# Optimization experiments

Hardware: AMD Instinct MI355X
Metric: run time of the kernel (lower is better)

## Reference

```python
import jax, jax.numpy as jnp
import numpy as np

B, E, H, W = 8, 256, 128, 128
E0 = E1 = E2 = E3 = E // 4  # channel_split=[2,2,2,2] -> equal quarters


def _dwconv(x, w, b, dilation, padding):
    # x: [B,C,H,W], w: [C,1,kh,kw] (OIHW, feature_group_count=C), b: [C]
    C = x.shape[1]
    y = jax.lax.conv_general_dilated(
        x, w,
        window_strides=(1, 1),
        padding=[(padding, padding), (padding, padding)],
        rhs_dilation=(dilation, dilation),
        feature_group_count=C,
        dimension_numbers=("NCHW", "OIHW", "NCHW"))
    return y + b[None, :, None, None]


def setup_inputs() -> dict:
    key = jax.random.key(0)
    ks = jax.random.split(key, 9)
    s = 0.05
    return {
        "x": jax.random.normal(ks[0], (B, E, H, W), dtype=jnp.float32),
        "w0": jax.random.normal(ks[1], (E, 1, 3, 3), dtype=jnp.float32) * s,
        "b0": jax.random.normal(ks[2], (E,), dtype=jnp.float32) * s,
        "w1": jax.random.normal(ks[3], (E1, 1, 3, 3), dtype=jnp.float32) * s,
        "b1": jax.random.normal(ks[4], (E1,), dtype=jnp.float32) * s,
        "w2": jax.random.normal(ks[5], (E2, 1, 5, 5), dtype=jnp.float32) * s,
        "b2": jax.random.normal(ks[6], (E2,), dtype=jnp.float32) * s,
        "w_pw": jax.random.normal(ks[7], (E, E), dtype=jnp.float32) * s,
        "b_pw": jax.random.normal(ks[8], (E,), dtype=jnp.float32) * s,
    }


def reference(x, w0, b0, w1, b1, w2, b2, w_pw, b_pw):
    # Stage 1: full-width 3x3 depthwise, dilation 1, padding 1
    x0 = _dwconv(x, w0, b0, dilation=1, padding=1)
    # Branch convs on channel slices of x0 (note: original code applies
    # DW_conv2 to BOTH the 3rd and 4th slices; DW_conv3 is never used).
    x1 = _dwconv(x0[:, E0:E0 + E1], w1, b1, dilation=3, padding=3)          # 3x3 dil3
    x2 = _dwconv(x0[:, E0 + E1:E0 + E1 + E2], w2, b2, dilation=3, padding=6)  # 5x5 dil3
    x3 = _dwconv(x0[:, E - E3:], w2, b2, dilation=3, padding=6)             # reuses DW_conv2
    xc = jnp.concatenate([x0[:, :E0], x1, x2, x3], axis=1)  # [B,E,H,W]
    # 1x1 pointwise conv as a channel GEMM
    y = jnp.einsum("bchw,oc->bohw", xc, w_pw) + b_pw[None, :, None, None]
    return y
```

## Files before the change

kernel.cpp:

```cpp
#include <hip/hip_runtime.h>

typedef _Float16 f16;
typedef _Float16 f16x8 __attribute__((ext_vector_type(8)));
typedef unsigned short u16x8 __attribute__((ext_vector_type(8)));
typedef float f32x4 __attribute__((ext_vector_type(4)));

#define GLB_AS(p) ((const __attribute__((address_space(1))) unsigned int*)(p))
#define LDS_AS(p) ((__attribute__((address_space(3))) unsigned int*)(p))

__global__ __launch_bounds__(256) void whalf(const float* __restrict__ w,
                                             f16* __restrict__ wh) {
  int i = blockIdx.x * 256 + threadIdx.x;
  wh[i] = (f16)w[i];
}

template <int HT>
__global__ __launch_bounds__(256) void dwfuse(
    const float* __restrict__ x, const float* __restrict__ w0,
    const float* __restrict__ b0, const float* __restrict__ w1,
    const float* __restrict__ b1, const float* __restrict__ w2,
    const float* __restrict__ b2, f16* __restrict__ Xp) {
  constexpr int S2 = 32 + 2 * HT;
  constexpr int S1 = S2 + 2;
  constexpr int PO = (HT == 6) ? 2 : 0;
  constexpr int QW = (S2 + 3) / 4;
  constexpr int LW = 52;
  __shared__ float xs[S1 * LW];
  __shared__ float ts[S2 * LW];
  const int tid = threadIdx.x;

  int b, ch;
  if constexpr (HT == 0) { b = blockIdx.z >> 6; ch = (int)(blockIdx.z & 63); }
  else if constexpr (HT == 3) { b = blockIdx.z >> 6; ch = 64 + (int)(blockIdx.z & 63); }
  else { b = blockIdx.z >> 7; ch = 128 + (int)(blockIdx.z & 127); }
  const int plane = b * 256 + ch;
  const int R0 = (int)blockIdx.y * 32, C0 = (int)blockIdx.x * 32;
  const float* xp = x + (size_t)plane * 16384;

  float W0[9];
#pragma unroll
  for (int k = 0; k < 9; ++k) W0[k] = w0[ch * 9 + k];
  const float B0 = b0[ch];

  const int br = R0 - HT - 1, bc = C0 - HT - 1;
  for (int i = tid; i < S1 * S1; i += 256) {
    int r = i / S1, c = i - r * S1;
    int gr = br + r, gc = bc + c;
    float v = 0.f;
    if ((unsigned)gr < 128u && (unsigned)gc < 128u) v = xp[gr * 128 + gc];
    xs[r * LW + c] = v;
  }
  __syncthreads();

  for (int q = tid; q < S2 * QW; q += 256) {
    int r = q / QW, c4 = (q - r * QW) * 4;
    float a0 = 0, a1 = 0, a2 = 0, a3 = 0;
#pragma unroll
    for (int dy = 0; dy < 3; ++dy) {
      const float* row = &xs[(r + dy) * LW + c4];
      float4 qa = *(const float4*)row;
      float4 qb = *(const float4*)(row + 4);
      float wA = W0[dy * 3 + 0], wB = W0[dy * 3 + 1], wC = W0[dy * 3 + 2];
      a0 += wA * qa.x + wB * qa.y + wC * qa.z;
      a1 += wA * qa.y + wB * qa.z + wC * qa.w;
      a2 += wA * qa.z + wB * qa.w + wC * qb.x;
      a3 += wA * qa.w + wB * qb.x + wC * qb.y;
    }
    int gr = R0 - HT + r;
    int gc = C0 - HT + c4;
    bool rok = (unsigned)gr < 128u;
    float o0 = (rok && (unsigned)(gc + 0) < 128u) ? a0 + B0 : 0.f;
    float o1 = (rok && (unsigned)(gc + 1) < 128u) ? a1 + B0 : 0.f;
    float o2 = (rok && (unsigned)(gc + 2) < 128u) ? a2 + B0 : 0.f;
    float o3 = (rok && (unsigned)(gc + 3) < 128u) ? a3 + B0 : 0.f;
    float* tp = &ts[r * LW + c4 + PO];
    tp[0] = o0; tp[1] = o1; tp[2] = o2; tp[3] = o3;
  }
  __syncthreads();

  const int orow = tid >> 3;
  const int oc4 = (tid & 7) << 2;
  float o0, o1, o2, o3;
  if constexpr (HT == 0) {
    float4 qa = *(const float4*)&ts[orow * LW + oc4];
    o0 = qa.x; o1 = qa.y; o2 = qa.z; o3 = qa.w;
  } else if constexpr (HT == 3) {
    const int wi = ch & 63;
    float W1[9];
#pragma unroll
    for (int k = 0; k < 9; ++k) W1[k] = w1[wi * 9 + k];
    o0 = o1 = o2 = o3 = b1[wi];
#pragma unroll
    for (int dy = 0; dy < 3; ++dy) {
      const float* row = &ts[(orow + 3 * dy) * LW + oc4];
      float4 qa = *(const float4*)row;
      float4 qb = *(const float4*)(row + 4);
      float4 qc = *(const float4*)(row + 8);
      float v[12] = {qa.x, qa.y, qa.z, qa.w, qb.x, qb.y, qb.z, qb.w,
                     qc.x, qc.y, qc.z, qc.w};
#pragma unroll
      for (int dx = 0; dx < 3; ++dx) {
        float w = W1[dy * 3 + dx];
        o0 += w * v[3 * dx + 0];
        o1 += w * v[3 * dx + 1];
        o2 += w * v[3 * dx + 2];
        o3 += w * v[3 * dx + 3];
      }
    }
  } else {
    const int wi = ch & 63;
    float W2[25];
#pragma unroll
    for (int k = 0; k < 25; ++k) W2[k] = w2[wi * 25 + k];
    o0 = o1 = o2 = o3 = b2[wi];
#pragma unroll
    for (int dy = 0; dy < 5; ++dy) {
      const float* row = &ts[(orow + 3 * dy) * LW + oc4];
      float4 qa = *(const float4*)(row + 0);
      float4 qb = *(const float4*)(row + 4);
      float4 qc = *(const float4*)(row + 8);
      float4 qd = *(const float4*)(row + 12);
      float4 qe = *(const float4*)(row + 16);
      float v[20] = {qa.x, qa.y, qa.z, qa.w, qb.x, qb.y, qb.z, qb.w,
                     qc.x, qc.y, qc.z, qc.w, qd.x, qd.y, qd.z, qd.w,
                     qe.x, qe.y, qe.z, qe.w};
#pragma unroll
      for (int dx = 0; dx < 5; ++dx) {
        float w = W2[dy * 5 + dx];
        o0 += w * v[3 * dx + 2];
        o1 += w * v[3 * dx + 3];
        o2 += w * v[3 * dx + 4];
        o3 += w * v[3 * dx + 5];
      }
    }
  }
  const size_t oidx =
      (size_t)plane * 16384 + (size_t)(R0 + orow) * 128 + (C0 + oc4);
  union { f16 h[4]; uint2 u; } ph;
  ph.h[0] = (f16)o0; ph.h[1] = (f16)o1; ph.h[2] = (f16)o2; ph.h[3] = (f16)o3;
  *(uint2*)&Xp[oidx] = ph.u;
}

__global__ __launch_bounds__(256) void t_xpose(const f16* __restrict__ Xp,
                                               f16* __restrict__ XT) {
  __shared__ unsigned ld[64 * 65];
  const int t = threadIdx.x;
  const int b = (int)blockIdx.z, c0 = (int)blockIdx.y << 6,
            p0 = (int)blockIdx.x << 6;
  {
    const int r = t >> 2, ch = (t & 3) << 4;
    const f16* src = Xp + (((size_t)b * 256 + c0 + r) << 14) + p0 + ch;
    u16x8 v0 = *(const u16x8*)src;
    u16x8 v1 = *(const u16x8*)(src + 8);
#pragma unroll
    for (int i = 0; i < 8; ++i) ld[r * 65 + ch + i] = v0[i];
#pragma unroll
    for (int i = 0; i < 8; ++i) ld[r * 65 + ch + 8 + i] = v1[i];
  }
  __syncthreads();
  {
    const int pr = t >> 2, cc = (t & 3) << 4;
    u16x8 w0, w1;
#pragma unroll
    for (int i = 0; i < 8; ++i) w0[i] = (unsigned short)ld[(cc + i) * 65 + pr];
#pragma unroll
    for (int i = 0; i < 8; ++i)
      w1[i] = (unsigned short)ld[(cc + 8 + i) * 65 + pr];
    f16* dst = XT + (((size_t)b * 16384 + p0 + pr) << 8) + c0 + cc;
    *(u16x8*)dst = w0;
    *(u16x8*)(dst + 8) = w1;
  }
}

__global__ __launch_bounds__(256) void pwgemm(const f16* __restrict__ XT,
                                              const f16* __restrict__ Wh,
                                              const float* __restrict__ bpw,
                                              float* __restrict__ out) {
  __shared__ f16 smem[16384];
  const int tid = threadIdx.x, lane = tid & 63, wid = tid >> 6;
  const int bx = (int)blockIdx.x;
  const int nblk = bx >> 1;
  const int m0 = (bx & 1) << 7;
  const int bb = nblk >> 7;
  const int p0 = (nblk & 127) << 7;

  const int spx = tid >> 3;
  const int so = (tid & 7) ^ (spx & 7);
  const f16* xb = XT + (((size_t)bb * 16384 + p0 + spx) << 8) + so * 8;
  const unsigned lwb =
      __builtin_amdgcn_readfirstlane((unsigned)(wid * 1024));

  const int wo = (wid >> 1) << 6, wp = (wid & 1) << 6;
  const int brow_ = lane & 15, boct = lane >> 4;
  const f16* wrow = Wh + (m0 + wo + brow_) * 256 + boct * 8;

  unsigned aoff[4][2];
#pragma unroll
  for (int mf = 0; mf < 4; ++mf) {
    int px = wp + mf * 16 + (lane & 15);
#pragma unroll
    for (int k2 = 0; k2 < 2; ++k2)
      aoff[mf][k2] =
          (unsigned)(px * 128 + ((((k2 << 2) + boct) ^ (px & 7)) << 4));
  }

  f32x4 acc[4][4] = {};

#pragma unroll
  for (int rnd = 0; rnd < 4; ++rnd)
    __builtin_amdgcn_global_load_lds(
        GLB_AS(xb + rnd * 8192),
        LDS_AS((char*)smem + rnd * 4096 + lwb), 16, 0, 0);
  __syncthreads();

  for (int ks = 0; ks < 4; ++ks) {
    const int cur = ks & 1;
    if (ks < 3) {
#pragma unroll
      for (int rnd = 0; rnd < 4; ++rnd)
        __builtin_amdgcn_global_load_lds(
            GLB_AS(xb + rnd * 8192 + (ks + 1) * 64),
            LDS_AS((char*)smem + (cur ^ 1) * 16384 + rnd * 4096 + lwb), 16, 0,
            0);
    }
    f16x8 bw[4][2], ax[4][2];
#pragma unroll
    for (int nf = 0; nf < 4; ++nf)
#pragma unroll
      for (int k2 = 0; k2 < 2; ++k2)
        bw[nf][k2] = *(const f16x8*)(wrow + nf * 16 * 256 + ks * 64 + k2 * 32);
#pragma unroll
    for (int mf = 0; mf < 4; ++mf)
#pragma unroll
      for (int k2 = 0; k2 < 2; ++k2)
        ax[mf][k2] =
            *(const f16x8*)((const char*)smem + cur * 16384 + aoff[mf][k2]);

#pragma unroll
    for (int k2 = 0; k2 < 2; ++k2)
#pragma unroll
      for (int mf = 0; mf < 4; ++mf)
#pragma unroll
        for (int nf = 0; nf < 4; ++nf)
          acc[mf][nf] = __builtin_amdgcn_mfma_f32_16x16x32_f16(
              ax[mf][k2], bw[nf][k2], acc[mf][nf], 0, 0, 0);
    __syncthreads();
  }

  float bias_o[4];
#pragma unroll
  for (int nf = 0; nf < 4; ++nf)
    bias_o[nf] = bpw[m0 + wo + nf * 16 + (lane & 15)];

  float* op = out + (size_t)bb * 4194304;
  const int px0 = p0 + wp + ((lane >> 4) << 2);
#pragma unroll
  for (int mf = 0; mf < 4; ++mf) {
#pragma unroll
    for (int nf = 0; nf < 4; ++nf) {
      const int o = m0 + wo + nf * 16 + (lane & 15);
      float4 v;
      v.x = acc[mf][nf][0] + bias_o[nf];
      v.y = acc[mf][nf][1] + bias_o[nf];
      v.z = acc[mf][nf][2] + bias_o[nf];
      v.w = acc[mf][nf][3] + bias_o[nf];
      *(float4*)&op[(size_t)o * 16384 + px0 + mf * 16] = v;
    }
  }
}

extern "C" void kernel_launch(void* const* d_in, const int* in_sizes, int n_in,
                              void* d_out, int out_size, void* d_ws,
                              size_t ws_size, hipStream_t stream) {
  const float* x = (const float*)d_in[0];
  const float* w0 = (const float*)d_in[1];
  const float* b0 = (const float*)d_in[2];
  const float* w1 = (const float*)d_in[3];
  const float* b1 = (const float*)d_in[4];
  const float* w2 = (const float*)d_in[5];
  const float* b2 = (const float*)d_in[6];
  const float* wpw = (const float*)d_in[7];
  const float* bpw = (const float*)d_in[8];
  float* out = (float*)d_out;

  f16* Xp = (f16*)((char*)d_out + 67108864);
  f16* XT = (f16*)d_ws;
  f16* Wh = (f16*)((char*)d_ws + 67108864);

  whalf<<<256, 256, 0, stream>>>(wpw, Wh);
  dwfuse<0><<<dim3(4, 4, 512), 256, 0, stream>>>(x, w0, b0, w1, b1, w2, b2, Xp);
  dwfuse<3><<<dim3(4, 4, 512), 256, 0, stream>>>(x, w0, b0, w1, b1, w2, b2, Xp);
  dwfuse<6><<<dim3(4, 4, 1024), 256, 0, stream>>>(x, w0, b0, w1, b1, w2, b2,
                                                  Xp);
  t_xpose<<<dim3(256, 4, 8), 256, 0, stream>>>(Xp, XT);
  pwgemm<<<2048, 256, 0, stream>>>(XT, Wh, bpw, out);
}
```

Baseline: 425.7 us.

## Simplify depthwise stages to scalar per-pixel loops and remap GEMM block order

Rewrites the fused depthwise kernel to compute one output pixel per thread iteration, using scalar LDS reads in place of float4 row loads with four outputs per thread. Outputs are now written as scalar f16 stores rather than packed 4-wide stores. The pointwise GEMM block index is also remapped so consecutive launched blocks are spread in strides of eight, likely to line up with the MI355X's eight XCDs and improve L2 locality. The scalar path issues more LDS reads and narrower global stores, which may add cost.

```diff
diff --git a/kernel.cpp b/kernel.cpp
--- a/kernel.cpp
+++ b/kernel.cpp
@@ -22,8 +22,6 @@
     const float* __restrict__ b2, f16* __restrict__ Xp) {
   constexpr int S2 = 32 + 2 * HT;
   constexpr int S1 = S2 + 2;
-  constexpr int PO = (HT == 6) ? 2 : 0;
-  constexpr int QW = (S2 + 3) / 4;
   constexpr int LW = 52;
   __shared__ float xs[S1 * LW];
   __shared__ float ts[S2 * LW];
@@ -52,93 +50,67 @@
   }
   __syncthreads();
 
-  for (int q = tid; q < S2 * QW; q += 256) {
-    int r = q / QW, c4 = (q - r * QW) * 4;
-    float a0 = 0, a1 = 0, a2 = 0, a3 = 0;
-#pragma unroll
-    for (int dy = 0; dy < 3; ++dy) {
-      const float* row = &xs[(r + dy) * LW + c4];
-      float4 qa = *(const float4*)row;
-      float4 qb = *(const float4*)(row + 4);
-      float wA = W0[dy * 3 + 0], wB = W0[dy * 3 + 1], wC = W0[dy * 3 + 2];
-      a0 += wA * qa.x + wB * qa.y + wC * qa.z;
-      a1 += wA * qa.y + wB * qa.z + wC * qa.w;
-      a2 += wA * qa.z + wB * qa.w + wC * qb.x;
-      a3 += wA * qa.w + wB * qb.x + wC * qb.y;
-    }
-    int gr = R0 - HT + r;
-    int gc = C0 - HT + c4;
-    bool rok = (unsigned)gr < 128u;
-    float o0 = (rok && (unsigned)(gc + 0) < 128u) ? a0 + B0 : 0.f;
-    float o1 = (rok && (unsigned)(gc + 1) < 128u) ? a1 + B0 : 0.f;
-    float o2 = (rok && (unsigned)(gc + 2) < 128u) ? a2 + B0 : 0.f;
-    float o3 = (rok && (unsigned)(gc + 3) < 128u) ? a3 + B0 : 0.f;
-    float* tp = &ts[r * LW + c4 + PO];
-    tp[0] = o0; tp[1] = o1; tp[2] = o2; tp[3] = o3;
-  }
-  __syncthreads();
-
-  const int orow = tid >> 3;
-  const int oc4 = (tid & 7) << 2;
-  float o0, o1, o2, o3;
+  for (int i = tid; i < S2 * S2; i += 256) {
+    int r = i / S2, c = i - r * S2;
+    const float* base = &xs[r * LW + c];
+    float a = B0;
+#pragma unroll
+    for (int dy = 0; dy < 3; ++dy)
+#pragma unroll
+      for (int dx = 0; dx < 3; ++dx) a += W0[dy * 3 + dx] * base[dy * LW + dx];
+    int gr = R0 - HT + r, gc = C0 - HT + c;
+    float o = ((unsigned)gr < 128u && (unsigned)gc < 128u) ? a : 0.f;
+    ts[r * LW + c] = o;
+  }
+  __syncthreads();
+
   if constexpr (HT == 0) {
-    float4 qa = *(const float4*)&ts[orow * LW + oc4];
-    o0 = qa.x; o1 = qa.y; o2 = qa.z; o3 = qa.w;
+#pragma unroll
+    for (int k = 0; k < 4; ++k) {
+      int i = tid + k * 256;
+      int r = i >> 5, c = i & 31;
+      float o = ts[r * LW + c];
+      Xp[(size_t)plane * 16384 + (size_t)(R0 + r) * 128 + (C0 + c)] = (f16)o;
+    }
   } else if constexpr (HT == 3) {
     const int wi = ch & 63;
     float W1[9];
 #pragma unroll
     for (int k = 0; k < 9; ++k) W1[k] = w1[wi * 9 + k];
-    o0 = o1 = o2 = o3 = b1[wi];
-#pragma unroll
-    for (int dy = 0; dy < 3; ++dy) {
-      const float* row = &ts[(orow + 3 * dy) * LW + oc4];
-      float4 qa = *(const float4*)row;
-      float4 qb = *(const float4*)(row + 4);
-      float4 qc = *(const float4*)(row + 8);
-      float v[12] = {qa.x, qa.y, qa.z, qa.w, qb.x, qb.y, qb.z, qb.w,
-                     qc.x, qc.y, qc.z, qc.w};
-#pragma unroll
-      for (int dx = 0; dx < 3; ++dx) {
-        float w = W1[dy * 3 + dx];
-        o0 += w * v[3 * dx + 0];
-        o1 += w * v[3 * dx + 1];
-        o2 += w * v[3 * dx + 2];
-        o3 += w * v[3 * dx + 3];
-      }
+    const float B1 = b1[wi];
+#pragma unroll
+    for (int k = 0; k < 4; ++k) {
+      int i = tid + k * 256;
+      int r = i >> 5, c = i & 31;
+      const float* base = &ts[r * LW + c];
+      float o = B1;
+#pragma unroll
+      for (int dy = 0; dy < 3; ++dy)
+#pragma unroll
+        for (int dx = 0; dx < 3; ++dx)
+          o += W1[dy * 3 + dx] * base[3 * dy * LW + 3 * dx];
+      Xp[(size_t)plane * 16384 + (size_t)(R0 + r) * 128 + (C0 + c)] = (f16)o;
     }
   } else {
     const int wi = ch & 63;
     float W2[25];
 #pragma unroll
     for (int k = 0; k < 25; ++k) W2[k] = w2[wi * 25 + k];
-    o0 = o1 = o2 = o3 = b2[wi];
-#pragma unroll
-    for (int dy = 0; dy < 5; ++dy) {
-      const float* row = &ts[(orow + 3 * dy) * LW + oc4];
-      float4 qa = *(const float4*)(row + 0);
-      float4 qb = *(const float4*)(row + 4);
-      float4 qc = *(const float4*)(row + 8);
-      float4 qd = *(const float4*)(row + 12);
-      float4 qe = *(const float4*)(row + 16);
-      float v[20] = {qa.x, qa.y, qa.z, qa.w, qb.x, qb.y, qb.z, qb.w,
-                     qc.x, qc.y, qc.z, qc.w, qd.x, qd.y, qd.z, qd.w,
-                     qe.x, qe.y, qe.z, qe.w};
-#pragma unroll
-      for (int dx = 0; dx < 5; ++dx) {
-        float w = W2[dy * 5 + dx];
-        o0 += w * v[3 * dx + 2];
-        o1 += w * v[3 * dx + 3];
-        o2 += w * v[3 * dx + 4];
-        o3 += w * v[3 * dx + 5];
-      }
-    }
-  }
-  const size_t oidx =
-      (size_t)plane * 16384 + (size_t)(R0 + orow) * 128 + (C0 + oc4);
-  union { f16 h[4]; uint2 u; } ph;
-  ph.h[0] = (f16)o0; ph.h[1] = (f16)o1; ph.h[2] = (f16)o2; ph.h[3] = (f16)o3;
-  *(uint2*)&Xp[oidx] = ph.u;
+    const float B2 = b2[wi];
+#pragma unroll
+    for (int k = 0; k < 4; ++k) {
+      int i = tid + k * 256;
+      int r = i >> 5, c = i & 31;
+      const float* base = &ts[r * LW + c];
+      float o = B2;
+#pragma unroll
+      for (int dy = 0; dy < 5; ++dy)
+#pragma unroll
+        for (int dx = 0; dx < 5; ++dx)
+          o += W2[dy * 5 + dx] * base[3 * dy * LW + 3 * dx];
+      Xp[(size_t)plane * 16384 + (size_t)(R0 + r) * 128 + (C0 + c)] = (f16)o;
+    }
+  }
 }
 
 __global__ __launch_bounds__(256) void t_xpose(const f16* __restrict__ Xp,
@@ -178,9 +150,10 @@
                                               float* __restrict__ out) {
   __shared__ f16 smem[16384];
   const int tid = threadIdx.x, lane = tid & 63, wid = tid >> 6;
-  const int bx = (int)blockIdx.x;
-  const int nblk = bx >> 1;
-  const int m0 = (bx & 1) << 7;
+  const int bid = (int)blockIdx.x;
+  const int wg = ((bid & 7) << 8) + (bid >> 3);
+  const int nblk = wg >> 1;
+  const int m0 = (wg & 1) << 7;
   const int bb = nblk >> 7;
   const int p0 = (nblk & 127) << 7;
 
```

Result: faster. 399.4 us (-6.2%).
